# Kernel optimization log

Measured on AMD Instinct MI355X. Metric: run time of the kernel, lower is better.

The kernel has to match this reference:

```python
import jax, jax.numpy as jnp
import numpy as np

NUM_HEADS = 16
HEAD_DIM = 128
ROPE_BASE = 10000.0


def rotate_half(x):
    x1, x2 = jnp.split(x, 2, axis=-1)
    return jnp.concatenate((-x2, x1), axis=-1)


def rope_cos_sin(seq_len, dim, dtype):
    inv_freq = 1.0 / (ROPE_BASE ** (jnp.arange(0, dim, 2, dtype=jnp.float32) / dim))
    t = jnp.arange(seq_len, dtype=jnp.float32)
    freqs = jnp.einsum('i,j->ij', t, inv_freq)          # [S, dim/2]
    emb = jnp.concatenate((freqs, freqs), axis=-1)       # [S, dim]
    return emb.astype(dtype)  # caller applies cos/sin


def setup_inputs() -> dict:
    key = jax.random.key(0)
    k0, k1, k2, k3, k4 = jax.random.split(key, 5)
    B, S, H = 2, 2048, 2048
    hd = H // NUM_HEADS
    scale = 0.02
    return {
        'hidden_states': jax.random.normal(k0, (B, S, H), dtype=jnp.float32),
        'Wq': jax.random.normal(k1, (H, H), dtype=jnp.float32) * scale,
        'Wk': jax.random.normal(k2, (hd, H), dtype=jnp.float32) * scale,
        'Wv': jax.random.normal(k3, (hd, H), dtype=jnp.float32) * scale,
        'Wo': jax.random.normal(k4, (H, H), dtype=jnp.float32) * scale,
    }


def reference(hidden_states, Wq, Wk, Wv, Wo):
    B, S, H = hidden_states.shape
    nH, hd = NUM_HEADS, HEAD_DIM

    # projections (torch Linear: x @ W.T)
    q = jnp.einsum('bsh,oh->bso', hidden_states, Wq).reshape(B, S, nH, hd)
    q = q.transpose(0, 2, 1, 3)                          # [B, nH, S, hd]
    k = jnp.einsum('bsh,dh->bsd', hidden_states, Wk)      # [B, S, hd] single KV head
    v = jnp.einsum('bsh,dh->bsd', hidden_states, Wv)      # [B, S, hd]

    # rotary embedding
    emb = rope_cos_sin(S, hd, hidden_states.dtype)        # [S, hd]
    cos, sin = jnp.cos(emb), jnp.sin(emb)
    q = q * cos[None, None] + rotate_half(q) * sin[None, None]
    k = k * cos[None] + rotate_half(k) * sin[None]

    # attention: Q heads against shared K/V head
    scores = jnp.einsum('bhqd,bkd->bhqk', q, k) / jnp.sqrt(jnp.asarray(hd, hidden_states.dtype))
    attn = jax.nn.softmax(scores, axis=-1)               # dropout is identity in eval
    out = jnp.einsum('bhqk,bkd->bhqd', attn, v)           # [B, nH, S, hd]
    out = out.transpose(0, 2, 1, 3).reshape(B, S, H)
    attn_output = jnp.einsum('bsh,oh->bso', out, Wo)

    # cache tensors returned by the torch module: k, v with head dim of 1
    return attn_output, k[:, None], v[:, None]
```

## Files before the change

### kernel.cpp

```cpp
#include <hip/hip_runtime.h>
#include <hip/hip_bf16.h>

typedef __hip_bfloat16 bf16;

#define NH   16
#define HD   128
#define SEQ  2048
#define BB   2
#define HID  2048

#define ROPE_C 0.14391156856f

using frag   = __attribute__((ext_vector_type(8))) short;
using f32x4  = __attribute__((ext_vector_type(4))) float;
using f32x16 = __attribute__((ext_vector_type(16))) float;


__device__ __forceinline__ void cvt8_store(const float4 f0, const float4 f1, bf16* dst) {
    union { frag v; bf16 h[8]; } p;
    p.h[0] = __float2bfloat16(f0.x); p.h[1] = __float2bfloat16(f0.y);
    p.h[2] = __float2bfloat16(f0.z); p.h[3] = __float2bfloat16(f0.w);
    p.h[4] = __float2bfloat16(f1.x); p.h[5] = __float2bfloat16(f1.y);
    p.h[6] = __float2bfloat16(f1.z); p.h[7] = __float2bfloat16(f1.w);
    *reinterpret_cast<frag*>(dst) = p.v;
}

__device__ __forceinline__ unsigned pk2(float a, float b) {
    union { bf16 h[2]; unsigned u; } p;
    p.h[0] = __float2bfloat16(a);
    p.h[1] = __float2bfloat16(b);
    return p.u;
}

__global__ __launch_bounds__(512) void gemm_qkv(const float* __restrict__ A,
                                                const float* __restrict__ Wq,
                                                const float* __restrict__ Wk,
                                                const float* __restrict__ Wv,
                                                bf16* __restrict__ qout,
                                                float* __restrict__ Ck,
                                                float* __restrict__ Cv,
                                                bf16* __restrict__ kb,
                                                bf16* __restrict__ vt) {
    __shared__ bf16 Asl[4096];
    __shared__ bf16 Bsl[4096];
    const int tid  = threadIdx.x;
    const int wave = tid >> 6;
    const int lane = tid & 63;
    const int quad = lane >> 4;
    const int l15  = lane & 15;
    const int row0 = blockIdx.y * 128;
    const int bx   = blockIdx.x;
    const bool isq  = bx < 16;
    const bool is_v = (bx == 17);
    const float* W  = isq ? Wq : (is_v ? Wv : Wk);
    const int col0  = isq ? bx * 128 : 0;

    const int sr = tid >> 2;
    const int sc = (tid & 3) * 8;

    f32x4 acc[8];
#pragma unroll
    for (int j = 0; j < 8; ++j) acc[j] = (f32x4){0.f,0.f,0.f,0.f};

    for (int k0 = 0; k0 < HID; k0 += 32) {
        __syncthreads();
        {
            const float4* a0 = reinterpret_cast<const float4*>(A + (size_t)(row0 + sr) * HID + k0 + sc);
            const float4* b0 = reinterpret_cast<const float4*>(W + (size_t)(col0 + sr) * HID + k0 + sc);
            cvt8_store(a0[0], a0[1], &Asl[tid * 8]);
            cvt8_store(b0[0], b0[1], &Bsl[tid * 8]);
        }
        __syncthreads();
        frag af, bfr[8];
        af = *reinterpret_cast<const frag*>(&Asl[(((wave*16 + l15)*4) + quad) * 8]);
#pragma unroll
        for (int j = 0; j < 8; ++j)
            bfr[j] = *reinterpret_cast<const frag*>(&Bsl[(((j*16 + l15)*4) + quad) * 8]);
#pragma unroll
        for (int j = 0; j < 8; ++j)
            acc[j] = __builtin_amdgcn_mfma_f32_16x16x32_bf16(af, bfr[j], acc[j], 0, 0, 0);
    }

    if (isq) {
#pragma unroll
        for (int r = 0; r < 4; ++r) {
            const int row = row0 + wave*16 + quad*4 + r;
            const int s = row & (SEQ - 1);
            bf16* crow = qout + (size_t)row * HID + col0;
#pragma unroll
            for (int j = 0; j < 4; ++j) {
                const int d = 16*j + l15;
                const float invf = expf(-(float)d * ROPE_C);
                float sn, cs;
                sincosf((float)s * invf, &sn, &cs);
                const float x1 = acc[j][r], x2 = acc[j+4][r];
                crow[d]      = __float2bfloat16(x1*cs - x2*sn);
                crow[d + 64] = __float2bfloat16(x2*cs + x1*sn);
            }
        }
    } else if (is_v) {
#pragma unroll
        for (int r = 0; r < 4; ++r) {
            const int row = row0 + wave*16 + quad*4 + r;
            const int s = row & (SEQ - 1);
            const int b = row >> 11;
            float* crow = Cv + (size_t)row * HD;
#pragma unroll
            for (int j = 0; j < 8; ++j) {
                const int d = 16*j + l15;
                const float val = acc[j][r];
                crow[d] = val;
                vt[((size_t)b * HD + d) * SEQ + s] = __float2bfloat16(val);
            }
        }
    } else {
#pragma unroll
        for (int r = 0; r < 4; ++r) {
            const int row = row0 + wave*16 + quad*4 + r;
            const int s = row & (SEQ - 1);
            float* crow = Ck + (size_t)row * HD;
#pragma unroll
            for (int j = 0; j < 4; ++j) {
                const int d = 16*j + l15;
                const float invf = expf(-(float)d * ROPE_C);
                float sn, cs;
                sincosf((float)s * invf, &sn, &cs);
                const float y1 = acc[j][r]*cs - acc[j+4][r]*sn;
                const float y2 = acc[j+4][r]*cs + acc[j][r]*sn;
                crow[d]      = y1;
                crow[d + 64] = y2;
                kb[(size_t)row * HD + d]      = __float2bfloat16(y1);
                kb[(size_t)row * HD + d + 64] = __float2bfloat16(y2);
            }
        }
    }
}

__global__ __launch_bounds__(128) void attn_mfma(const bf16* __restrict__ qbuf,
                                                 const bf16* __restrict__ kb,
                                                 const bf16* __restrict__ vt,
                                                 bf16* __restrict__ attn_out) {
    __shared__ bf16 Ks[8192];
    __shared__ bf16 Vt[8192];

    const int tid  = threadIdx.x;
    const int wave = tid >> 6;
    const int lane = tid & 63;
    const int l31  = lane & 31;
    const int h    = lane >> 5;
    const int q0   = blockIdx.x * 64;
    const int hh   = blockIdx.y;
    const int b    = blockIdx.z;

    const bf16* kbb = kb + (size_t)b * SEQ * HD;
    const bf16* vtb = vt + (size_t)b * HD * SEQ;

    frag qfr[8];
    {
        const bf16* qrow = qbuf + ((size_t)(b * SEQ + q0 + wave * 32 + l31)) * HID + hh * HD;
#pragma unroll
        for (int c = 0; c < 8; ++c)
            qfr[c] = *reinterpret_cast<const frag*>(qrow + c * 16 + h * 8);
    }

    int koff[8], voff[8];
#pragma unroll
    for (int i = 0; i < 8; ++i) {
        const int n  = tid + i * 128;
        const int kl = (n >> 1) & 31, khs = n & 1;
        const int key  = ((n >> 9) << 5) + kl;
        const int dimb = (((n >> 6) & 7) << 4) + (khs << 3);
        koff[i] = key * HD + dimb;
        const int ks  = (n >> 6) & 3;
        const int dim = ((n >> 8) << 5) + kl;
        const int kA  = ((ks >> 1) << 5) + ((ks & 1) << 4) + (khs << 2);
        voff[i] = dim * SEQ + kA;
    }
    const int rpos = (l31 * 2 + h) * 16;

    f32x16 oacc[4];
#pragma unroll
    for (int dt = 0; dt < 4; ++dt)
#pragma unroll
        for (int r = 0; r < 16; ++r) oacc[dt][r] = 0.f;
    float mrow = -1e30f;
    float lrow = 0.f;
    const float scale = 0.088388347648318433f;

    for (int t0 = 0; t0 < SEQ; t0 += 64) {
        __syncthreads();
        {
            uint4 krg[8];
            const bf16* kt0 = kbb + (size_t)t0 * HD;
#pragma unroll
            for (int i = 0; i < 8; ++i)
                krg[i] = *reinterpret_cast<const uint4*>(kt0 + koff[i]);
#pragma unroll
            for (int i = 0; i < 8; ++i)
                *reinterpret_cast<uint4*>(reinterpret_cast<char*>(Ks) + (tid + i*128) * 16) = krg[i];
            uint4 vrg[8];
            const bf16* vt0 = vtb + t0;
#pragma unroll
            for (int i = 0; i < 8; ++i) {
                const uint2 a = *reinterpret_cast<const uint2*>(vt0 + voff[i]);
                const uint2 c = *reinterpret_cast<const uint2*>(vt0 + voff[i] + 8);
                vrg[i] = (uint4){a.x, a.y, c.x, c.y};
            }
#pragma unroll
            for (int i = 0; i < 8; ++i)
                *reinterpret_cast<uint4*>(reinterpret_cast<char*>(Vt) + (tid + i*128) * 16) = vrg[i];
        }
        __syncthreads();

        f32x16 sacc[2];
#pragma unroll
        for (int kt = 0; kt < 2; ++kt)
#pragma unroll
            for (int r = 0; r < 16; ++r) sacc[kt][r] = 0.f;
#pragma unroll
        for (int c = 0; c < 8; ++c) {
            const frag kf0 = *reinterpret_cast<const frag*>(
                reinterpret_cast<const char*>(Ks) + (0*8 + c) * 1024 + rpos);
            const frag kf1 = *reinterpret_cast<const frag*>(
                reinterpret_cast<const char*>(Ks) + (1*8 + c) * 1024 + rpos);
            sacc[0] = __builtin_amdgcn_mfma_f32_32x32x16_bf16(kf0, qfr[c], sacc[0], 0, 0, 0);
            sacc[1] = __builtin_amdgcn_mfma_f32_32x32x16_bf16(kf1, qfr[c], sacc[1], 0, 0, 0);
        }

        float mx = -1e30f;
#pragma unroll
        for (int kt = 0; kt < 2; ++kt)
#pragma unroll
            for (int r = 0; r < 16; ++r) mx = fmaxf(mx, sacc[kt][r]);
        mx = fmaxf(mx, __shfl_xor(mx, 32));
        const bool skip = (bool)__all(mx - mrow <= 90.0f);
        const float mn = skip ? mrow : fmaxf(mrow, mx);
        const float al = skip ? 1.f : __expf((mrow - mn) * scale);
        float p[2][16];
        float ps = 0.f;
#pragma unroll
        for (int kt = 0; kt < 2; ++kt)
#pragma unroll
            for (int r = 0; r < 16; ++r) {
                p[kt][r] = __expf((sacc[kt][r] - mn) * scale);
                ps += p[kt][r];
            }
        ps += __shfl_xor(ps, 32);
        lrow = lrow * al + ps;
        mrow = mn;

        frag pb[4];
#pragma unroll
        for (int ks = 0; ks < 4; ++ks) {
            const int kt = ks >> 1, ta = (ks & 1) * 2, tb = ta + 1;
            union { unsigned u[4]; frag f; } pf;
            pf.u[0] = pk2(p[kt][ta*4+0], p[kt][ta*4+1]);
            pf.u[1] = pk2(p[kt][ta*4+2], p[kt][ta*4+3]);
            pf.u[2] = pk2(p[kt][tb*4+0], p[kt][tb*4+1]);
            pf.u[3] = pk2(p[kt][tb*4+2], p[kt][tb*4+3]);
            pb[ks] = pf.f;
        }

        if (!skip)
#pragma unroll
            for (int dt = 0; dt < 4; ++dt)
#pragma unroll
                for (int r = 0; r < 16; ++r) oacc[dt][r] *= al;

#pragma unroll
        for (int dt = 0; dt < 4; ++dt) {
#pragma unroll
            for (int ks = 0; ks < 4; ++ks) {
                const frag vf = *reinterpret_cast<const frag*>(
                    reinterpret_cast<const char*>(Vt) + (dt*4 + ks) * 1024 + rpos);
                oacc[dt] = __builtin_amdgcn_mfma_f32_32x32x16_bf16(vf, pb[ks], oacc[dt], 0, 0, 0);
            }
        }
    }

    {
        const float inv = 1.f / lrow;
        const int s = q0 + wave * 32 + l31;
        bf16* orow = attn_out + ((size_t)(b * SEQ + s)) * HID + hh * HD;
#pragma unroll
        for (int dt = 0; dt < 4; ++dt)
#pragma unroll
            for (int t = 0; t < 4; ++t) {
                uint2 val;
                val.x = pk2(oacc[dt][t*4+0] * inv, oacc[dt][t*4+1] * inv);
                val.y = pk2(oacc[dt][t*4+2] * inv, oacc[dt][t*4+3] * inv);
                *reinterpret_cast<uint2*>(orow + dt*32 + t*8 + h*4) = val;
            }
    }
}

__global__ __launch_bounds__(512) void gemm_o_mfma(const bf16* __restrict__ A,
                                                   const float* __restrict__ W,
                                                   float* __restrict__ C) {
    __shared__ bf16 Asl[4096];
    __shared__ bf16 Bsl[4096];
    const int tid  = threadIdx.x;
    const int wave = tid >> 6;
    const int lane = tid & 63;
    const int quad = lane >> 4;
    const int l15  = lane & 15;
    const int row0 = blockIdx.y * 128;
    const int col0 = blockIdx.x * 128;

    const int sr = tid >> 2;
    const int sc = (tid & 3) * 8;

    f32x4 acc[8];
#pragma unroll
    for (int j = 0; j < 8; ++j) acc[j] = (f32x4){0.f,0.f,0.f,0.f};

    for (int k0 = 0; k0 < HID; k0 += 32) {
        __syncthreads();
        {
            *reinterpret_cast<uint4*>(&Asl[tid * 8]) =
                *reinterpret_cast<const uint4*>(A + (size_t)(row0 + sr) * HID + k0 + sc);
            const float4* b0 = reinterpret_cast<const float4*>(W + (size_t)(col0 + sr) * HID + k0 + sc);
            cvt8_store(b0[0], b0[1], &Bsl[tid * 8]);
        }
        __syncthreads();
        frag af, bfr[8];
        af = *reinterpret_cast<const frag*>(&Asl[(((wave*16 + l15)*4) + quad) * 8]);
#pragma unroll
        for (int j = 0; j < 8; ++j)
            bfr[j] = *reinterpret_cast<const frag*>(&Bsl[(((j*16 + l15)*4) + quad) * 8]);
#pragma unroll
        for (int j = 0; j < 8; ++j)
            acc[j] = __builtin_amdgcn_mfma_f32_16x16x32_bf16(af, bfr[j], acc[j], 0, 0, 0);
    }

#pragma unroll
    for (int r = 0; r < 4; ++r) {
        const int row = row0 + wave*16 + quad*4 + r;
        float* crow = C + (size_t)row * HID + col0;
#pragma unroll
        for (int j = 0; j < 8; ++j)
            crow[16*j + l15] = acc[j][r];
    }
}

extern "C" void kernel_launch(void* const* d_in, const int* in_sizes, int n_in,
                              void* d_out, int out_size, void* d_ws, size_t ws_size,
                              hipStream_t stream) {
    const float* hs = (const float*)d_in[0];
    const float* Wq = (const float*)d_in[1];
    const float* Wk = (const float*)d_in[2];
    const float* Wv = (const float*)d_in[3];
    const float* Wo = (const float*)d_in[4];

    float* out      = (float*)d_out;
    float* out_attn = out;
    float* out_k    = out + 8388608;
    float* out_v    = out + 8388608 + 524288;

    bf16* qbuf = (bf16*)d_out;
    bf16* kb   = (bf16*)((char*)d_out + 16777216);
    bf16* vt   = (bf16*)((char*)d_out + 17825792);
    bf16* attn_out = (bf16*)d_ws;

    gemm_qkv  <<<dim3(18, (BB*SEQ)/128), dim3(512), 0, stream>>>(hs, Wq, Wk, Wv,
                                                                 qbuf, out_k, out_v, kb, vt);
    attn_mfma <<<dim3(SEQ/64, NH, BB),   dim3(128), 0, stream>>>(qbuf, kb, vt, attn_out);
    gemm_o_mfma<<<dim3(HID/128, (BB*SEQ)/128), dim3(512), 0, stream>>>(attn_out, Wo, out_attn);
}
```

Before: 433.9 us.

## Split attention key tiles across two wave groups with split-K softmax merge

The attention block grows from 2 to 4 waves. Each pair of waves handles half of every 64-key tile (32 keys), so each wave carries half the S accumulators and issues half the MFMAs per tile. Partial max, sum and output accumulators are merged through LDS at the end. LDS tiles for K and V are now XOR-swizzled to avoid bank conflicts. The cost is an extra reduction epilogue with several barriers, and each wave still keeps its own full O accumulator.

```diff
diff --git a/kernel.cpp b/kernel.cpp
--- a/kernel.cpp
+++ b/kernel.cpp
@@ -136,18 +136,19 @@
     }
 }
 
-__global__ __launch_bounds__(128) void attn_mfma(const bf16* __restrict__ qbuf,
+__global__ __launch_bounds__(256) void attn_mfma(const bf16* __restrict__ qbuf,
                                                  const bf16* __restrict__ kb,
                                                  const bf16* __restrict__ vt,
                                                  bf16* __restrict__ attn_out) {
-    __shared__ bf16 Ks[8192];
-    __shared__ bf16 Vt[8192];
+    __shared__ char lds[32768];
 
     const int tid  = threadIdx.x;
     const int wave = tid >> 6;
     const int lane = tid & 63;
     const int l31  = lane & 31;
     const int h    = lane >> 5;
+    const int qg   = wave & 1;
+    const int kg   = wave >> 1;
     const int q0   = blockIdx.x * 64;
     const int hh   = blockIdx.y;
     const int b    = blockIdx.z;
@@ -157,26 +158,38 @@
 
     frag qfr[8];
     {
-        const bf16* qrow = qbuf + ((size_t)(b * SEQ + q0 + wave * 32 + l31)) * HID + hh * HD;
+        const bf16* qrow = qbuf + ((size_t)(b * SEQ + q0 + qg * 32 + l31)) * HID + hh * HD;
 #pragma unroll
         for (int c = 0; c < 8; ++c)
             qfr[c] = *reinterpret_cast<const frag*>(qrow + c * 16 + h * 8);
     }
 
-    int koff[8], voff[8];
+    const int sl   = tid & 127;
+    const int kg_s = tid >> 7;
+
+    int klof[4];
+#pragma unroll
+    for (int i = 0; i < 4; ++i) {
+        const int n   = sl + i * 128;
+        const int key = n >> 4, d = (n >> 1) & 7, hs = n & 1;
+        const int L   = d * 64 + key * 2 + hs;
+        klof[i] = (kg_s * 8192 + L * 16) ^ (((((key >> 2) ^ d) & 7)) << 4);
+    }
+    int vlof[8], vgof[8];
 #pragma unroll
     for (int i = 0; i < 8; ++i) {
-        const int n  = tid + i * 128;
-        const int kl = (n >> 1) & 31, khs = n & 1;
-        const int key  = ((n >> 9) << 5) + kl;
-        const int dimb = (((n >> 6) & 7) << 4) + (khs << 3);
-        koff[i] = key * HD + dimb;
-        const int ks  = (n >> 6) & 3;
-        const int dim = ((n >> 8) << 5) + kl;
-        const int kA  = ((ks >> 1) << 5) + ((ks & 1) << 4) + (khs << 2);
-        voff[i] = dim * SEQ + kA;
-    }
+        const int g   = sl + i * 128;
+        const int dim = g >> 3, ks = (g >> 2) & 1, m = (g >> 1) & 1, hs = g & 1;
+        const int dt  = dim >> 5;
+        const int C   = (dt * 2 + ks) * 64 + (dim & 31) * 2 + hs;
+        const int B   = 16384 + kg_s * 8192 + C * 16 + m * 8;
+        const int xv  = (((dim & 31) >> 2) ^ (dt * 2 + ks)) & 7;
+        vlof[i] = B ^ (xv << 4);
+        vgof[i] = dim * SEQ + kg_s * 32 + (g & 7) * 4;
+    }
+
     const int rpos = (l31 * 2 + h) * 16;
+    const int rsw  = rpos ^ ((((rpos >> 7) & 7)) << 4);
 
     f32x16 oacc[4];
 #pragma unroll
@@ -187,77 +200,63 @@
     float lrow = 0.f;
     const float scale = 0.088388347648318433f;
 
-    for (int t0 = 0; t0 < SEQ; t0 += 64) {
+    for (int it = 0; it < SEQ / 64; ++it) {
         __syncthreads();
         {
-            uint4 krg[8];
-            const bf16* kt0 = kbb + (size_t)t0 * HD;
+            const bf16* kp = kbb + (size_t)it * 64 * HD + kg_s * 4096;
+            const bf16* vp = vtb + it * 64;
+            uint4 krg[4];
+            uint2 vrg[8];
+#pragma unroll
+            for (int i = 0; i < 4; ++i)
+                krg[i] = *reinterpret_cast<const uint4*>(kp + (sl + i * 128) * 8);
 #pragma unroll
             for (int i = 0; i < 8; ++i)
-                krg[i] = *reinterpret_cast<const uint4*>(kt0 + koff[i]);
+                vrg[i] = *reinterpret_cast<const uint2*>(vp + vgof[i]);
+#pragma unroll
+            for (int i = 0; i < 4; ++i)
+                *reinterpret_cast<uint4*>(lds + klof[i]) = krg[i];
 #pragma unroll
             for (int i = 0; i < 8; ++i)
-                *reinterpret_cast<uint4*>(reinterpret_cast<char*>(Ks) + (tid + i*128) * 16) = krg[i];
-            uint4 vrg[8];
-            const bf16* vt0 = vtb + t0;
-#pragma unroll
-            for (int i = 0; i < 8; ++i) {
-                const uint2 a = *reinterpret_cast<const uint2*>(vt0 + voff[i]);
-                const uint2 c = *reinterpret_cast<const uint2*>(vt0 + voff[i] + 8);
-                vrg[i] = (uint4){a.x, a.y, c.x, c.y};
-            }
-#pragma unroll
-            for (int i = 0; i < 8; ++i)
-                *reinterpret_cast<uint4*>(reinterpret_cast<char*>(Vt) + (tid + i*128) * 16) = vrg[i];
-        }
-        __syncthreads();
-
-        f32x16 sacc[2];
-#pragma unroll
-        for (int kt = 0; kt < 2; ++kt)
-#pragma unroll
-            for (int r = 0; r < 16; ++r) sacc[kt][r] = 0.f;
+                *reinterpret_cast<uint2*>(lds + vlof[i]) = vrg[i];
+        }
+        __syncthreads();
+
+        f32x16 sacc;
+#pragma unroll
+        for (int r = 0; r < 16; ++r) sacc[r] = 0.f;
 #pragma unroll
         for (int c = 0; c < 8; ++c) {
-            const frag kf0 = *reinterpret_cast<const frag*>(
-                reinterpret_cast<const char*>(Ks) + (0*8 + c) * 1024 + rpos);
-            const frag kf1 = *reinterpret_cast<const frag*>(
-                reinterpret_cast<const char*>(Ks) + (1*8 + c) * 1024 + rpos);
-            sacc[0] = __builtin_amdgcn_mfma_f32_32x32x16_bf16(kf0, qfr[c], sacc[0], 0, 0, 0);
-            sacc[1] = __builtin_amdgcn_mfma_f32_32x32x16_bf16(kf1, qfr[c], sacc[1], 0, 0, 0);
+            const frag kf = *reinterpret_cast<const frag*>(
+                lds + kg * 8192 + c * 1024 + (rsw ^ (c << 4)));
+            sacc = __builtin_amdgcn_mfma_f32_32x32x16_bf16(kf, qfr[c], sacc, 0, 0, 0);
         }
 
         float mx = -1e30f;
 #pragma unroll
-        for (int kt = 0; kt < 2; ++kt)
-#pragma unroll
-            for (int r = 0; r < 16; ++r) mx = fmaxf(mx, sacc[kt][r]);
+        for (int r = 0; r < 16; ++r) mx = fmaxf(mx, sacc[r]);
         mx = fmaxf(mx, __shfl_xor(mx, 32));
         const bool skip = (bool)__all(mx - mrow <= 90.0f);
         const float mn = skip ? mrow : fmaxf(mrow, mx);
         const float al = skip ? 1.f : __expf((mrow - mn) * scale);
-        float p[2][16];
+        float p[16];
         float ps = 0.f;
 #pragma unroll
-        for (int kt = 0; kt < 2; ++kt)
-#pragma unroll
-            for (int r = 0; r < 16; ++r) {
-                p[kt][r] = __expf((sacc[kt][r] - mn) * scale);
-                ps += p[kt][r];
-            }
+        for (int r = 0; r < 16; ++r) {
+            p[r] = __expf((sacc[r] - mn) * scale);
+            ps += p[r];
+        }
         ps += __shfl_xor(ps, 32);
         lrow = lrow * al + ps;
         mrow = mn;
 
-        frag pb[4];
-#pragma unroll
-        for (int ks = 0; ks < 4; ++ks) {
-            const int kt = ks >> 1, ta = (ks & 1) * 2, tb = ta + 1;
+        frag pb[2];
+#pragma unroll
+        for (int ks = 0; ks < 2; ++ks) {
             union { unsigned u[4]; frag f; } pf;
-            pf.u[0] = pk2(p[kt][ta*4+0], p[kt][ta*4+1]);
-            pf.u[1] = pk2(p[kt][ta*4+2], p[kt][ta*4+3]);
-            pf.u[2] = pk2(p[kt][tb*4+0], p[kt][tb*4+1]);
-            pf.u[3] = pk2(p[kt][tb*4+2], p[kt][tb*4+3]);
+#pragma unroll
+            for (int w = 0; w < 4; ++w)
+                pf.u[w] = pk2(p[8 * ks + 2 * w], p[8 * ks + 2 * w + 1]);
             pb[ks] = pf.f;
         }
 
@@ -268,29 +267,61 @@
                 for (int r = 0; r < 16; ++r) oacc[dt][r] *= al;
 
 #pragma unroll
-        for (int dt = 0; dt < 4; ++dt) {
-#pragma unroll
-            for (int ks = 0; ks < 4; ++ks) {
+        for (int dt = 0; dt < 4; ++dt)
+#pragma unroll
+            for (int ks = 0; ks < 2; ++ks) {
+                const int cb = dt * 2 + ks;
                 const frag vf = *reinterpret_cast<const frag*>(
-                    reinterpret_cast<const char*>(Vt) + (dt*4 + ks) * 1024 + rpos);
+                    lds + 16384 + kg * 8192 + cb * 1024 + (rsw ^ (cb << 4)));
                 oacc[dt] = __builtin_amdgcn_mfma_f32_32x32x16_bf16(vf, pb[ks], oacc[dt], 0, 0, 0);
             }
-        }
-    }
-
-    {
-        const float inv = 1.f / lrow;
-        const int s = q0 + wave * 32 + l31;
-        bf16* orow = attn_out + ((size_t)(b * SEQ + s)) * HID + hh * HD;
-#pragma unroll
-        for (int dt = 0; dt < 4; ++dt)
+    }
+
+    __syncthreads();
+    float* fl = reinterpret_cast<float*>(lds);
+    if (h == 0) {
+        fl[(qg * 2 + kg) * 32 + l31]       = mrow;
+        fl[128 + (qg * 2 + kg) * 32 + l31] = lrow;
+    }
+    __syncthreads();
+    const float m0 = fl[qg * 64 + l31],       m1 = fl[qg * 64 + 32 + l31];
+    const float l0 = fl[128 + qg * 64 + l31], l1 = fl[128 + qg * 64 + 32 + l31];
+    const float ms = fmaxf(m0, m1);
+    const float c0 = __expf((m0 - ms) * scale);
+    const float c1 = __expf((m1 - ms) * scale);
+    const float inv = 1.f / (c0 * l0 + c1 * l1);
+    const float cs = kg ? c1 : c0;
+#pragma unroll
+    for (int dt = 0; dt < 4; ++dt)
+#pragma unroll
+        for (int r = 0; r < 16; ++r) oacc[dt][r] *= cs;
+
+    float* ob = reinterpret_cast<float*>(lds + 1024);
+#pragma unroll
+    for (int dt = 0; dt < 4; ++dt) {
+        __syncthreads();
+        if (kg == 1) {
+            float* dst = ob + (qg * 64 + lane) * 17;
+#pragma unroll
+            for (int r = 0; r < 16; ++r) dst[r] = oacc[dt][r];
+        }
+        __syncthreads();
+        if (kg == 0) {
+            const float* sp = ob + (qg * 64 + lane) * 17;
+            const int s = q0 + qg * 32 + l31;
+            bf16* orow = attn_out + ((size_t)(b * SEQ + s)) * HID + hh * HD;
 #pragma unroll
             for (int t = 0; t < 4; ++t) {
+                const float v0 = (oacc[dt][t*4+0] + sp[t*4+0]) * inv;
+                const float v1 = (oacc[dt][t*4+1] + sp[t*4+1]) * inv;
+                const float v2 = (oacc[dt][t*4+2] + sp[t*4+2]) * inv;
+                const float v3 = (oacc[dt][t*4+3] + sp[t*4+3]) * inv;
                 uint2 val;
-                val.x = pk2(oacc[dt][t*4+0] * inv, oacc[dt][t*4+1] * inv);
-                val.y = pk2(oacc[dt][t*4+2] * inv, oacc[dt][t*4+3] * inv);
-                *reinterpret_cast<uint2*>(orow + dt*32 + t*8 + h*4) = val;
+                val.x = pk2(v0, v1);
+                val.y = pk2(v2, v3);
+                *reinterpret_cast<uint2*>(orow + dt * 32 + t * 8 + h * 4) = val;
             }
+        }
     }
 }
 
@@ -364,6 +395,6 @@
 
     gemm_qkv  <<<dim3(18, (BB*SEQ)/128), dim3(512), 0, stream>>>(hs, Wq, Wk, Wv,
                                                                  qbuf, out_k, out_v, kb, vt);
-    attn_mfma <<<dim3(SEQ/64, NH, BB),   dim3(128), 0, stream>>>(qbuf, kb, vt, attn_out);
+    attn_mfma <<<dim3(SEQ/64, NH, BB),   dim3(256), 0, stream>>>(qbuf, kb, vt, attn_out);
     gemm_o_mfma<<<dim3(HID/128, (BB*SEQ)/128), dim3(512), 0, stream>>>(attn_out, Wo, out_attn);
 }
```

Result: faster. 392.0 us (-9.7%).
